# Performance work log

Hardware: AMD Instinct MI355X
Metric: run time of the kernel (lower is better)

## Reference

```python
import jax, jax.numpy as jnp
import numpy as np

B, D, N_CLASSES = 8192, 256, 64
MARGIN = 0.5


def setup_inputs() -> dict:
    key = jax.random.key(0)
    k1, k2 = jax.random.split(key)
    emb = jax.random.normal(k1, (B, D), dtype=jnp.float32)
    emb = emb / jnp.linalg.norm(emb, axis=1, keepdims=True)  # module expects L2-normalised
    labels = jax.random.randint(k2, (B,), 0, N_CLASSES)
    return {"embeddings": emb, "labels": labels}


def _pairwise_dist(x):
    # torch.cdist(x, x, p=2): sqrt of clamped squared distances, safe at 0 for grads
    sq = jnp.sum(x * x, axis=1)
    d2 = jnp.maximum(sq[:, None] + sq[None, :] - 2.0 * (x @ x.T), 0.0)
    safe = jnp.where(d2 > 0.0, d2, 1.0)
    return jnp.where(d2 > 0.0, jnp.sqrt(safe), 0.0)


def reference(embeddings, labels):
    # Vectorized semi-hard mining: for each anchor,
    #   d_ap = max positive distance; the mined negative is the MIN negative
    #   distance (argmin over the semi-hard subset == global neg argmin when
    #   that min is < d_ap + margin; otherwise the subset is empty -> skip).
    dist = _pairwise_dist(embeddings)            # [B, B]
    n = labels.shape[0]
    same = labels[:, None] == labels[None, :]
    eye = jnp.eye(n, dtype=bool)
    pos_mask = same & ~eye
    neg_mask = ~same

    NEG = jnp.float32(-1e30)
    POS = jnp.float32(1e30)
    d_ap = jnp.max(jnp.where(pos_mask, dist, NEG), axis=1)   # hardest positive
    d_an = jnp.min(jnp.where(neg_mask, dist, POS), axis=1)   # closest negative

    has_pos = jnp.any(pos_mask, axis=1)
    has_neg = jnp.any(neg_mask, axis=1)
    valid = has_pos & has_neg & (d_an < d_ap + MARGIN)       # semi-hard exists

    losses = jax.nn.relu(d_ap - d_an + MARGIN)
    count = jnp.sum(valid)
    total = jnp.sum(jnp.where(valid, losses, 0.0))
    zero = jnp.sum(embeddings) * 0.0
    return jnp.where(count > 0, total / jnp.maximum(count, 1).astype(losses.dtype), zero)
```

## Files before the change

### kernel.cpp

```cpp
#include <hip/hip_runtime.h>
#include <hip/hip_bf16.h>

#define Bn 8192
#define Dn 256
#define MARGIN_F 0.5f

typedef short short8 __attribute__((ext_vector_type(8)));
typedef float floatx4 __attribute__((ext_vector_type(4)));

__device__ inline unsigned short f2bf(float f) {
    unsigned int u = __float_as_uint(f);
    unsigned int r = (u + 0x7fffu + ((u >> 16) & 1u)) >> 16;
    return (unsigned short)r;
}

#define OFF_SQ   ((size_t)Bn * Dn * 2)
#define OFF_POS  (OFF_SQ + Bn * 4)
#define OFF_NEG  (OFF_POS + Bn * 4)
#define OFF_ACC  (OFF_NEG + Bn * 4)

__global__ __launch_bounds__(256) void prep_kernel(
        const float* __restrict__ emb, unsigned short* __restrict__ embT,
        float* __restrict__ sq, unsigned int* __restrict__ posb,
        unsigned int* __restrict__ negb, unsigned int* __restrict__ accs) {
    const int w = threadIdx.x >> 6;
    const int lane = threadIdx.x & 63;
    const int row = blockIdx.x * 4 + w;

    const float4 v = *(const float4*)(emb + (size_t)row * Dn + lane * 4);
    float ss = v.x * v.x + v.y * v.y + v.z * v.z + v.w * v.w;
    #pragma unroll
    for (int m = 32; m >= 1; m >>= 1) ss += __shfl_xor(ss, m);

    uint2 o;
    o.x = (unsigned int)f2bf(v.x) | ((unsigned int)f2bf(v.y) << 16);
    o.y = (unsigned int)f2bf(v.z) | ((unsigned int)f2bf(v.w) << 16);
    const int kg = lane >> 1;
    *(uint2*)(embT + ((size_t)kg * Bn + row) * 8 + (lane & 1) * 4) = o;

    if (lane == 0) {
        sq[row] = ss;
        posb[row] = 0u;
        negb[row] = 0xFFFFFFFFu;
    }
    if (blockIdx.x == 0 && threadIdx.x == 0) {
        accs[0] = 0u; accs[1] = 0u; accs[2] = 0u;
    }
}

__global__ __launch_bounds__(256, 2) void mine_kernel(
        const unsigned short* __restrict__ embT, const float* __restrict__ sq,
        const int* __restrict__ labels, unsigned int* __restrict__ posb,
        unsigned int* __restrict__ negb) {
    const int tid  = threadIdx.x;
    const int w    = tid >> 6;
    const int lane = tid & 63;
    const int quad = lane >> 4;
    const int c    = lane & 15;

    const int iBase  = blockIdx.x * 256 + w * 64;
    const int jSplit = blockIdx.y * 512;

    const size_t KS = (size_t)4 * Bn * 8;

    short8 aFrag[4][8];
    #pragma unroll
    for (int m = 0; m < 4; ++m) {
        const unsigned short* ap = embT + ((size_t)quad * Bn + iBase + m * 16 + c) * 8;
        #pragma unroll
        for (int ks = 0; ks < 8; ++ks)
            aFrag[m][ks] = *(const short8*)(ap + ks * KS);
    }
    int labI[4][4];
    #pragma unroll
    for (int m = 0; m < 4; ++m)
        #pragma unroll
        for (int r = 0; r < 4; ++r)
            labI[m][r] = labels[iBase + m * 16 + quad * 4 + r];

    float rpos[4][4], rneg[4][4];
    #pragma unroll
    for (int m = 0; m < 4; ++m)
        #pragma unroll
        for (int r = 0; r < 4; ++r) { rpos[m][r] = -1e30f; rneg[m][r] = 1e30f; }

    for (int jt = 0; jt < 16; ++jt) {
        #pragma unroll
        for (int n = 0; n < 2; ++n) {
            const int jRow = jSplit + jt * 32 + n * 16 + c;
            const unsigned short* bp = embT + ((size_t)quad * Bn + jRow) * 8;
            const float sj = sq[jRow];
            const int   lj = labels[jRow];
            floatx4 acc[4];
            #pragma unroll
            for (int m = 0; m < 4; ++m) acc[m] = (floatx4){0.f, 0.f, 0.f, 0.f};
            #pragma unroll
            for (int kc = 0; kc < 2; ++kc) {
                short8 bF[4];
                #pragma unroll
                for (int k4 = 0; k4 < 4; ++k4)
                    bF[k4] = *(const short8*)(bp + (kc * 4 + k4) * KS);
                #pragma unroll
                for (int k4 = 0; k4 < 4; ++k4)
                    #pragma unroll
                    for (int m = 0; m < 4; ++m)
                        acc[m] = __builtin_amdgcn_mfma_f32_16x16x32_bf16(
                            aFrag[m][kc * 4 + k4], bF[k4], acc[m], 0, 0, 0);
            }
            #pragma unroll
            for (int m = 0; m < 4; ++m)
                #pragma unroll
                for (int r = 0; r < 4; ++r) {
                    float s = fmaf(-2.0f, acc[m][r], sj);
                    bool  e = (lj == labI[m][r]);
                    rpos[m][r] = e ? fmaxf(rpos[m][r], s) : rpos[m][r];
                    rneg[m][r] = e ? rneg[m][r] : fminf(rneg[m][r], s);
                }
        }
    }

    #pragma unroll
    for (int m = 0; m < 4; ++m)
        #pragma unroll
        for (int r = 0; r < 4; ++r) {
            float p = rpos[m][r], q = rneg[m][r];
            #pragma unroll
            for (int msk = 1; msk <= 8; msk <<= 1) {
                p = fmaxf(p, __shfl_xor(p, msk));
                q = fminf(q, __shfl_xor(q, msk));
            }
            if (c == 0) {
                int ig = iBase + m * 16 + quad * 4 + r;
                if (p > -1e29f) atomicMax(&posb[ig], __float_as_uint(p + 4.0f));
                if (q <  1e29f) atomicMin(&negb[ig], __float_as_uint(q + 4.0f));
            }
        }
}

__global__ __launch_bounds__(256) void finalize_kernel(
        const float* __restrict__ sq, const unsigned int* __restrict__ posb,
        const unsigned int* __restrict__ negb, float* __restrict__ accsF,
        unsigned int* __restrict__ accsU, float* __restrict__ out) {
    const int i = blockIdx.x * 256 + threadIdx.x;
    unsigned int pb = posb[i], nb = negb[i];
    bool hp = (pb != 0u);
    bool hn = (nb != 0xFFFFFFFFu);
    float si  = sq[i];
    float dap = sqrtf(fmaxf(si + (__uint_as_float(pb) - 4.0f), 0.0f));
    float dan = sqrtf(fmaxf(si + (__uint_as_float(nb) - 4.0f), 0.0f));
    bool valid = hp && hn && (dan < dap + MARGIN_F);
    float t  = valid ? fmaxf(dap - dan + MARGIN_F, 0.0f) : 0.0f;
    float cc = valid ? 1.0f : 0.0f;
    #pragma unroll
    for (int m = 32; m >= 1; m >>= 1) {
        t  += __shfl_xor(t, m);
        cc += __shfl_xor(cc, m);
    }
    __shared__ float sT[4], sC[4];
    int w = threadIdx.x >> 6, lane = threadIdx.x & 63;
    if (lane == 0) { sT[w] = t; sC[w] = cc; }
    __syncthreads();
    if (threadIdx.x == 0) {
        atomicAdd(&accsF[0], sT[0] + sT[1] + sT[2] + sT[3]);
        atomicAdd(&accsF[1], sC[0] + sC[1] + sC[2] + sC[3]);
        __threadfence();
        unsigned int ticket = atomicAdd(&accsU[2], 1u);
        if (ticket == gridDim.x - 1) {
            float tot = atomicAdd(&accsF[0], 0.0f);
            float cnt = atomicAdd(&accsF[1], 0.0f);
            out[0] = (cnt > 0.0f) ? tot / cnt : 0.0f;
        }
    }
}

extern "C" void kernel_launch(void* const* d_in, const int* in_sizes, int n_in,
                              void* d_out, int out_size, void* d_ws, size_t ws_size,
                              hipStream_t stream) {
    const float* emb   = (const float*)d_in[0];
    const int*  labels = (const int*)d_in[1];
    float* out = (float*)d_out;

    char* ws = (char*)d_ws;
    unsigned short* embT = (unsigned short*)ws;
    float*        sqv  = (float*)(ws + OFF_SQ);
    unsigned int* posb = (unsigned int*)(ws + OFF_POS);
    unsigned int* negb = (unsigned int*)(ws + OFF_NEG);
    float*        accsF = (float*)(ws + OFF_ACC);
    unsigned int* accsU = (unsigned int*)(ws + OFF_ACC);

    prep_kernel<<<Bn / 4, 256, 0, stream>>>(emb, embT, sqv, posb, negb, accsU);
    mine_kernel<<<dim3(32, 16), 256, 0, stream>>>(embT, sqv, labels, posb, negb);
    finalize_kernel<<<Bn / 256, 256, 0, stream>>>(sqv, posb, negb, accsF, accsU, out);
}
```

Baseline: 118.7 us.

## Shrink mine_kernel tiles to one 16-row MFMA tile per wave for occupancy

```diff
diff --git a/kernel.cpp b/kernel.cpp
--- a/kernel.cpp
+++ b/kernel.cpp
@@ -48,7 +48,7 @@
     }
 }
 
-__global__ __launch_bounds__(256, 2) void mine_kernel(
+__global__ __launch_bounds__(256, 4) void mine_kernel(
         const unsigned short* __restrict__ embT, const float* __restrict__ sq,
         const int* __restrict__ labels, unsigned int* __restrict__ posb,
         unsigned int* __restrict__ negb) {
@@ -58,83 +58,66 @@
     const int quad = lane >> 4;
     const int c    = lane & 15;
 
-    const int iBase  = blockIdx.x * 256 + w * 64;
+    const int iBase  = blockIdx.x * 64 + w * 16;
     const int jSplit = blockIdx.y * 512;
 
     const size_t KS = (size_t)4 * Bn * 8;
 
-    short8 aFrag[4][8];
-    #pragma unroll
-    for (int m = 0; m < 4; ++m) {
-        const unsigned short* ap = embT + ((size_t)quad * Bn + iBase + m * 16 + c) * 8;
+    short8 aFrag[8];
+    {
+        const unsigned short* ap = embT + ((size_t)quad * Bn + iBase + c) * 8;
         #pragma unroll
         for (int ks = 0; ks < 8; ++ks)
-            aFrag[m][ks] = *(const short8*)(ap + ks * KS);
+            aFrag[ks] = *(const short8*)(ap + ks * KS);
     }
-    int labI[4][4];
+    int labI[4];
     #pragma unroll
-    for (int m = 0; m < 4; ++m)
+    for (int r = 0; r < 4; ++r)
+        labI[r] = labels[iBase + quad * 4 + r];
+
+    float rpos[4], rneg[4];
+    #pragma unroll
+    for (int r = 0; r < 4; ++r) { rpos[r] = -1e30f; rneg[r] = 1e30f; }
+
+    for (int step = 0; step < 32; ++step) {
+        const int jRow = jSplit + step * 16 + c;
+        const unsigned short* bp = embT + ((size_t)quad * Bn + jRow) * 8;
+        const float sj = sq[jRow];
+        const int   lj = labels[jRow];
+
+        short8 bF[8];
         #pragma unroll
-        for (int r = 0; r < 4; ++r)
-            labI[m][r] = labels[iBase + m * 16 + quad * 4 + r];
+        for (int ks = 0; ks < 8; ++ks)
+            bF[ks] = *(const short8*)(bp + ks * KS);
 
-    float rpos[4][4], rneg[4][4];
-    #pragma unroll
-    for (int m = 0; m < 4; ++m)
+        floatx4 acc = {0.f, 0.f, 0.f, 0.f};
         #pragma unroll
-        for (int r = 0; r < 4; ++r) { rpos[m][r] = -1e30f; rneg[m][r] = 1e30f; }
+        for (int ks = 0; ks < 8; ++ks)
+            acc = __builtin_amdgcn_mfma_f32_16x16x32_bf16(aFrag[ks], bF[ks], acc, 0, 0, 0);
 
-    for (int jt = 0; jt < 16; ++jt) {
         #pragma unroll
-        for (int n = 0; n < 2; ++n) {
-            const int jRow = jSplit + jt * 32 + n * 16 + c;
-            const unsigned short* bp = embT + ((size_t)quad * Bn + jRow) * 8;
-            const float sj = sq[jRow];
-            const int   lj = labels[jRow];
-            floatx4 acc[4];
-            #pragma unroll
-            for (int m = 0; m < 4; ++m) acc[m] = (floatx4){0.f, 0.f, 0.f, 0.f};
-            #pragma unroll
-            for (int kc = 0; kc < 2; ++kc) {
-                short8 bF[4];
-                #pragma unroll
-                for (int k4 = 0; k4 < 4; ++k4)
-                    bF[k4] = *(const short8*)(bp + (kc * 4 + k4) * KS);
-                #pragma unroll
-                for (int k4 = 0; k4 < 4; ++k4)
-                    #pragma unroll
-                    for (int m = 0; m < 4; ++m)
-                        acc[m] = __builtin_amdgcn_mfma_f32_16x16x32_bf16(
-                            aFrag[m][kc * 4 + k4], bF[k4], acc[m], 0, 0, 0);
-            }
-            #pragma unroll
-            for (int m = 0; m < 4; ++m)
-                #pragma unroll
-                for (int r = 0; r < 4; ++r) {
-                    float s = fmaf(-2.0f, acc[m][r], sj);
-                    bool  e = (lj == labI[m][r]);
-                    rpos[m][r] = e ? fmaxf(rpos[m][r], s) : rpos[m][r];
-                    rneg[m][r] = e ? rneg[m][r] : fminf(rneg[m][r], s);
-                }
+        for (int r = 0; r < 4; ++r) {
+            float s = fmaf(-2.0f, acc[r], sj);
+            bool  e = (lj == labI[r]);
+            rpos[r] = e ? fmaxf(rpos[r], s) : rpos[r];
+            rneg[r] = e ? rneg[r] : fminf(rneg[r], s);
         }
     }
 
     #pragma unroll
-    for (int m = 0; m < 4; ++m)
+    for (int r = 0; r < 4; ++r) {
+        float p = rpos[r], q = rneg[r];
         #pragma unroll
-        for (int r = 0; r < 4; ++r) {
-            float p = rpos[m][r], q = rneg[m][r];
-            #pragma unroll
-            for (int msk = 1; msk <= 8; msk <<= 1) {
-                p = fmaxf(p, __shfl_xor(p, msk));
-                q = fminf(q, __shfl_xor(q, msk));
-            }
-            if (c == 0) {
-                int ig = iBase + m * 16 + quad * 4 + r;
-                if (p > -1e29f) atomicMax(&posb[ig], __float_as_uint(p + 4.0f));
-                if (q <  1e29f) atomicMin(&negb[ig], __float_as_uint(q + 4.0f));
-            }
+        for (int msk = 1; msk <= 8; msk <<= 1) {
+            p = fmaxf(p, __shfl_xor(p, msk));
+            q = fminf(q, __shfl_xor(q, msk));
         }
+        if (c == 0) {
+            int ig = iBase + quad * 4 + r;
+            if (p > -1e29f) atomicMax(&posb[ig], __float_as_uint(p + 4.0f));
+            if (q <  1e29f) atomicMin(&negb[ig], __float_as_uint(q + 4.0f));
+        }
+    }
 }
 
 __global__ __launch_bounds__(256) void finalize_kernel(
@@ -189,6 +172,6 @@
     unsigned int* accsU = (unsigned int*)(ws + OFF_ACC);
 
     prep_kernel<<<Bn / 4, 256, 0, stream>>>(emb, embT, sqv, posb, negb, accsU);
-    mine_kernel<<<dim3(32, 16), 256, 0, stream>>>(embT, sqv, labels, posb, negb);
+    mine_kernel<<<dim3(128, 16), 256, 0, stream>>>(embT, sqv, labels, posb, negb);
     finalize_kernel<<<Bn / 256, 256, 0, stream>>>(sqv, posb, negb, accsF, accsU, out);
 }
```

Result: slower. 143.6 us (+21.0%).
